# Kernel optimization log

Hardware: AMD Instinct MI355X
Metric: run time of the kernel (lower is better)

The kernel has to match this reference:

```python
import jax, jax.numpy as jnp
import numpy as np

DIM = 768
NUM_HEADS = 12
HEAD_DIM = DIM // NUM_HEADS
SCALE = HEAD_DIM ** -0.5  # qk_scale=None -> head_dim**-0.5


def setup_inputs() -> dict:
    key = jax.random.key(0)
    k1, k2, k3, k4 = jax.random.split(key, 4)
    B, N, C = 8, 1024, DIM
    x = jax.random.normal(k1, (B, N, C), dtype=jnp.float32)
    # qkv_bias=False -> no qkv bias; proj Linear has bias by default
    w_qkv = jax.random.normal(k2, (3 * C, C), dtype=jnp.float32) * (C ** -0.5)
    w_proj = jax.random.normal(k3, (C, C), dtype=jnp.float32) * (C ** -0.5)
    b_proj = jax.random.normal(k4, (C,), dtype=jnp.float32) * 0.02
    return {"x": x, "w_qkv": w_qkv, "w_proj": w_proj, "b_proj": b_proj}


def reference(x, w_qkv, w_proj, b_proj):
    B, N, C = x.shape
    H, D = NUM_HEADS, HEAD_DIM
    # qkv: [B,N,3C] -> [3,B,H,N,D]
    qkv = jnp.einsum('bnc,kc->bnk', x, w_qkv)
    qkv = qkv.reshape(B, N, 3, H, D).transpose(2, 0, 3, 1, 4)
    q, k, v = qkv[0], qkv[1], qkv[2]
    attn = jnp.einsum('bhnd,bhmd->bhnm', q, k) * SCALE
    attn = jax.nn.softmax(attn, axis=-1)  # attn_drop=0.0 -> identity
    out = jnp.einsum('bhnm,bhmd->bhnd', attn, v)
    out = out.transpose(0, 2, 1, 3).reshape(B, N, C)
    out = jnp.einsum('bnc,oc->bno', out, w_proj) + b_proj  # proj_drop=0.0
    return out
```

## Files before the change

### kernel.cpp

```cpp
#include <hip/hip_runtime.h>
#include <hip/hip_bf16.h>
#include <math.h>


typedef __bf16 bf16;
typedef __bf16 bf16x8 __attribute__((ext_vector_type(8)));
typedef __bf16 bf16x4 __attribute__((ext_vector_type(4)));
typedef float  f32x4  __attribute__((ext_vector_type(4)));
typedef short  s16x4  __attribute__((ext_vector_type(4)));

#define AS1 __attribute__((address_space(1)))
#define AS3 __attribute__((address_space(3)))

static __device__ __forceinline__ f32x4 mfma16x16x16bf16(s16x4 a, s16x4 b, f32x4 c) {
#if __has_builtin(__builtin_amdgcn_mfma_f32_16x16x16bf16_1k)
    return __builtin_amdgcn_mfma_f32_16x16x16bf16_1k(a, b, c, 0, 0, 0);
#else
    asm("v_mfma_f32_16x16x16_bf16 %0, %1, %2, %0" : "+v"(c) : "v"(a), "v"(b));
    return c;
#endif
}

__global__ void cvt3_f32_bf16(const float* __restrict__ s1, bf16* __restrict__ d1, int n1,
                              const float* __restrict__ s2, bf16* __restrict__ d2, int n2,
                              const float* __restrict__ s3, bf16* __restrict__ d3, int n3) {
    int i = blockIdx.x * blockDim.x + threadIdx.x;
    int stride = gridDim.x * blockDim.x;
    int total = n1 + n2 + n3;
    for (; i < total; i += stride) {
        const float* s; bf16* d; int k;
        if (i < n1)            { s = s1; d = d1; k = i; }
        else if (i < n1 + n2)  { s = s2; d = d2; k = i - n1; }
        else                   { s = s3; d = d3; k = i - n1 - n2; }
        f32x4 a = ((const f32x4*)s)[2 * (size_t)k];
        f32x4 bv = ((const f32x4*)s)[2 * (size_t)k + 1];
        bf16x8 o;
        o[0] = (bf16)a[0]; o[1] = (bf16)a[1]; o[2] = (bf16)a[2]; o[3] = (bf16)a[3];
        o[4] = (bf16)bv[0]; o[5] = (bf16)bv[1]; o[6] = (bf16)bv[2]; o[7] = (bf16)bv[3];
        ((bf16x8*)d)[k] = o;
    }
}

template <int EPI>
__launch_bounds__(256, 2)
__global__ void gemm_bt(const bf16* __restrict__ A, const bf16* __restrict__ Bw, int Kdim,
                        bf16* __restrict__ qo, bf16* __restrict__ ko, bf16* __restrict__ vto,
                        float* __restrict__ outf, const float* __restrict__ bias) {
    __shared__ alignas(16) bf16 As[2][128 * 64];
    __shared__ alignas(16) bf16 Bs[2][128 * 64];
    const int tid  = threadIdx.x;
    const int lane = tid & 63;
    const int wave = tid >> 6;
    const int lo = lane & 15, hi = lane >> 4;
    const int wr = wave >> 1, wc = wave & 1;
    const int m0 = blockIdx.x * 128;
    const int n0 = blockIdx.y * 128;

    const int s_phys = tid & 7;

    f32x4 acc[4][4] = {};

#define STAGE(buf, ks)                                                          \
    {                                                                           \
        _Pragma("unroll")                                                       \
        for (int i = 0; i < 4; ++i) {                                           \
            int row = ((i * 256 + tid) >> 3);                                   \
            int sl  = s_phys ^ (row & 7);                                       \
            __builtin_amdgcn_global_load_lds(                                   \
                (const AS1 void*)(A + (size_t)(m0 + row) * Kdim + (ks) * 64 + sl * 8), \
                (AS3 void*)(&As[buf][0] + (i * 256 + wave * 64) * 8), 16, 0, 0);\
            __builtin_amdgcn_global_load_lds(                                   \
                (const AS1 void*)(Bw + (size_t)(n0 + row) * Kdim + (ks) * 64 + sl * 8), \
                (AS3 void*)(&Bs[buf][0] + (i * 256 + wave * 64) * 8), 16, 0, 0);\
        }                                                                       \
    }

    const int KS = Kdim >> 6;
    STAGE(0, 0);
    __syncthreads();

    int cur = 0;
    for (int ks = 0; ks < KS; ++ks) {
        if (ks + 1 < KS) STAGE(cur ^ 1, ks + 1);

        bf16x8 af[4][2], bfr[4][2];
#pragma unroll
        for (int kk = 0; kk < 2; ++kk) {
            const int sl = ((kk << 2) | hi) ^ (lo & 7);
#pragma unroll
            for (int i = 0; i < 4; ++i)
                af[i][kk] = *(const bf16x8*)&As[cur][(wr * 64 + i * 16 + lo) * 64 + sl * 8];
#pragma unroll
            for (int j = 0; j < 4; ++j)
                bfr[j][kk] = *(const bf16x8*)&Bs[cur][(wc * 64 + j * 16 + lo) * 64 + sl * 8];
        }
#pragma unroll
        for (int i = 0; i < 4; ++i)
#pragma unroll
            for (int j = 0; j < 4; ++j) {
                acc[i][j] = __builtin_amdgcn_mfma_f32_16x16x32_bf16(af[i][0], bfr[j][0], acc[i][j], 0, 0, 0);
                acc[i][j] = __builtin_amdgcn_mfma_f32_16x16x32_bf16(af[i][1], bfr[j][1], acc[i][j], 0, 0, 0);
            }

        __syncthreads();
        cur ^= 1;
    }
#undef STAGE

    if (EPI == 0) {
        const int part = n0 / 768;
#pragma unroll
        for (int i = 0; i < 4; ++i) {
            int grow = m0 + wr * 64 + i * 16 + (hi << 2);
            int b = grow >> 10;
            int n = grow & 1023;
#pragma unroll
            for (int j = 0; j < 4; ++j) {
                int col = n0 + wc * 64 + j * 16 + lo;
                int rem = col - part * 768;
                int h = rem >> 6, d = rem & 63;
#pragma unroll
                for (int r = 0; r < 4; ++r) {
                    bf16 v = (bf16)acc[i][j][r];
                    int nn = n + r;
                    if (part == 0)
                        qo[((size_t)(b * 12 + h) * 1024 + nn) * 64 + d] = v;
                    else if (part == 1)
                        ko[((size_t)(b * 12 + h) * 1024 + nn) * 64 + d] = v;
                    else
                        vto[((size_t)(b * 12 + h) * 64 + d) * 1024 + nn] = v;
                }
            }
        }
    } else {
#pragma unroll
        for (int i = 0; i < 4; ++i) {
            int grow = m0 + wr * 64 + i * 16 + (hi << 2);
#pragma unroll
            for (int j = 0; j < 4; ++j) {
                int col = n0 + wc * 64 + j * 16 + lo;
                float bv = bias[col];
#pragma unroll
                for (int r = 0; r < 4; ++r)
                    outf[(size_t)(grow + r) * 768 + col] = acc[i][j][r] + bv;
            }
        }
    }
}

__launch_bounds__(256, 3)
__global__ void flash_attn(const bf16* __restrict__ qg, const bf16* __restrict__ kg,
                           const bf16* __restrict__ vtg, bf16* __restrict__ og) {
    __shared__ alignas(16) bf16 Ks[64 * 72];
    __shared__ alignas(16) bf16 Vts[64 * 72];

    const int tid = threadIdx.x, lane = tid & 63, wave = tid >> 6;
    const int lo = lane & 15, hi = lane >> 4;

    const int bid = blockIdx.x + (int)gridDim.x * blockIdx.y;
    const int xcd = bid & 7, idx = bid >> 3;
    const int head = xcd * 12 + (idx >> 3);
    const int q0 = (idx & 7) * 128;
    const int b = head / 12, h = head % 12;

    const size_t baseQK = (size_t)head * 1024 * 64;
    const size_t baseVt = (size_t)head * 64 * 1024;

    bf16x8 qf[2][2];
#pragma unroll
    for (int jq = 0; jq < 2; ++jq)
#pragma unroll
        for (int kk = 0; kk < 2; ++kk) {
            bf16x8 v = *(const bf16x8*)&qg[baseQK +
                (size_t)(q0 + wave * 32 + jq * 16 + lo) * 64 + kk * 32 + hi * 8];
#pragma unroll
            for (int e = 0; e < 8; ++e) v[e] = (bf16)((float)v[e] * 0.125f);
            qf[jq][kk] = v;
        }

    f32x4 of[4][2] = {};
    float lsum[2] = {0.f, 0.f};

    const int srow = tid >> 3;
    const int sc8  = (tid & 7) * 8;
    f32x4 kr[2], vr[2];

#pragma unroll
    for (int s = 0; s < 2; ++s) {
        kr[s] = *(const f32x4*)&kg[baseQK + (size_t)(srow + 32 * s) * 64 + sc8];
        vr[s] = *(const f32x4*)&vtg[baseVt + (size_t)(srow + 32 * s) * 1024 + sc8];
    }
#pragma unroll
    for (int s = 0; s < 2; ++s) {
        *(f32x4*)&Ks[(srow + 32 * s) * 72 + sc8]  = kr[s];
        *(f32x4*)&Vts[(srow + 32 * s) * 72 + sc8] = vr[s];
    }

    for (int t = 0; t < 16; ++t) {
        if (t + 1 < 16) {
#pragma unroll
            for (int s = 0; s < 2; ++s) {
                kr[s] = *(const f32x4*)&kg[baseQK +
                    (size_t)((t + 1) * 64 + srow + 32 * s) * 64 + sc8];
                vr[s] = *(const f32x4*)&vtg[baseVt +
                    (size_t)(srow + 32 * s) * 1024 + (t + 1) * 64 + sc8];
            }
        }
        __syncthreads();

        bf16x8 kf[4][2];
#pragma unroll
        for (int j = 0; j < 4; ++j)
#pragma unroll
            for (int kk = 0; kk < 2; ++kk)
                kf[j][kk] = *(const bf16x8*)&Ks[(j * 16 + lo) * 72 + kk * 32 + hi * 8];

        __builtin_amdgcn_s_setprio(1);
        f32x4 st[4][2];
#pragma unroll
        for (int j = 0; j < 4; ++j)
#pragma unroll
            for (int jq = 0; jq < 2; ++jq) {
                f32x4 z = {0.f, 0.f, 0.f, 0.f};
                z = __builtin_amdgcn_mfma_f32_16x16x32_bf16(kf[j][0], qf[jq][0], z, 0, 0, 0);
                st[j][jq] = __builtin_amdgcn_mfma_f32_16x16x32_bf16(kf[j][1], qf[jq][1], z, 0, 0, 0);
            }
        __builtin_amdgcn_s_setprio(0);

        s16x4 pb[4][2];
#pragma unroll
        for (int j = 0; j < 4; ++j)
#pragma unroll
            for (int jq = 0; jq < 2; ++jq) {
                f32x4 p;
#pragma unroll
                for (int r = 0; r < 4; ++r) p[r] = __expf(st[j][jq][r] - 10.0f);
                lsum[jq] += (p[0] + p[1]) + (p[2] + p[3]);
                bf16x4 pk;
#pragma unroll
                for (int r = 0; r < 4; ++r) pk[r] = (bf16)p[r];
                pb[j][jq] = __builtin_bit_cast(s16x4, pk);
            }

        __builtin_amdgcn_s_setprio(1);
#pragma unroll
        for (int jd = 0; jd < 4; ++jd) {
#pragma unroll
            for (int j = 0; j < 4; ++j) {
                s16x4 va = *(const s16x4*)&Vts[(jd * 16 + lo) * 72 + j * 16 + hi * 4];
#pragma unroll
                for (int jq = 0; jq < 2; ++jq)
                    of[jd][jq] = mfma16x16x16bf16(va, pb[j][jq], of[jd][jq]);
            }
        }
        __builtin_amdgcn_s_setprio(0);

        __syncthreads();
        if (t + 1 < 16) {
#pragma unroll
            for (int s = 0; s < 2; ++s) {
                *(f32x4*)&Ks[(srow + 32 * s) * 72 + sc8]  = kr[s];
                *(f32x4*)&Vts[(srow + 32 * s) * 72 + sc8] = vr[s];
            }
        }
    }

#pragma unroll
    for (int jq = 0; jq < 2; ++jq) {
        lsum[jq] += __shfl_xor(lsum[jq], 16);
        lsum[jq] += __shfl_xor(lsum[jq], 32);
    }

#pragma unroll
    for (int jq = 0; jq < 2; ++jq) {
        float rl = 1.0f / lsum[jq];
        int n = q0 + wave * 32 + jq * 16 + lo;
#pragma unroll
        for (int jd = 0; jd < 4; ++jd) {
            bf16x4 o;
#pragma unroll
            for (int r = 0; r < 4; ++r) o[r] = (bf16)(of[jd][jq][r] * rl);
            *(bf16x4*)&og[((size_t)b * 1024 + n) * 768 + h * 64 + jd * 16 + hi * 4] = o;
        }
    }
}

extern "C" void kernel_launch(void* const* d_in, const int* in_sizes, int n_in,
                              void* d_out, int out_size, void* d_ws, size_t ws_size,
                              hipStream_t stream) {
    const float* x      = (const float*)d_in[0];
    const float* w_qkv  = (const float*)d_in[1];
    const float* w_proj = (const float*)d_in[2];
    const float* b_proj = (const float*)d_in[3];
    float* out = (float*)d_out;

    bf16* xb     = (bf16*)d_ws;
    bf16* wqkvb  = xb + (size_t)8192 * 768;
    bf16* wprojb = wqkvb + (size_t)2304 * 768;
    bf16* qb     = wprojb + (size_t)768 * 768;
    bf16* kb     = qb + (size_t)96 * 1024 * 64;
    bf16* vtb    = kb + (size_t)96 * 1024 * 64;
    bf16* aob    = vtb + (size_t)96 * 1024 * 64;

    cvt3_f32_bf16<<<1024, 256, 0, stream>>>(x, xb, 8192 * 768 / 8,
                                            w_qkv, wqkvb, 2304 * 768 / 8,
                                            w_proj, wprojb, 768 * 768 / 8);

    gemm_bt<0><<<dim3(64, 18), 256, 0, stream>>>(xb, wqkvb, 768, qb, kb, vtb, nullptr, nullptr);
    flash_attn<<<dim3(8, 96), 256, 0, stream>>>(qb, kb, vtb, aob);
    gemm_bt<1><<<dim3(64, 6), 256, 0, stream>>>(aob, wprojb, 768, nullptr, nullptr, nullptr, out, b_proj);
}
```

Before: 200.4 us.

## Single-buffer GEMM LDS, raise occupancy, and remap blocks for XCD locality

The GEMM drops double-buffered shared memory in favour of a single buffer with a load-sync-compute-sync loop, halving LDS use so launch bounds can request four blocks per CU instead of two. The grid becomes 1D and block IDs are remapped so consecutive blocks on the same XCD share M-tiles, aiming for better L2 reuse. The cost is that global loads no longer overlap with MFMA work inside a block, so latency hiding now depends on having more resident blocks. The GY template parameter is unused.

```diff
diff --git a/kernel.cpp b/kernel.cpp
--- a/kernel.cpp
+++ b/kernel.cpp
@@ -41,26 +41,28 @@
     }
 }
 
-template <int EPI>
-__launch_bounds__(256, 2)
+template <int EPI, int GY>
+__launch_bounds__(256, 4)
 __global__ void gemm_bt(const bf16* __restrict__ A, const bf16* __restrict__ Bw, int Kdim,
                         bf16* __restrict__ qo, bf16* __restrict__ ko, bf16* __restrict__ vto,
                         float* __restrict__ outf, const float* __restrict__ bias) {
-    __shared__ alignas(16) bf16 As[2][128 * 64];
-    __shared__ alignas(16) bf16 Bs[2][128 * 64];
+    __shared__ alignas(16) bf16 As[128 * 64];
+    __shared__ alignas(16) bf16 Bs[128 * 64];
     const int tid  = threadIdx.x;
     const int lane = tid & 63;
     const int wave = tid >> 6;
     const int lo = lane & 15, hi = lane >> 4;
     const int wr = wave >> 1, wc = wave & 1;
-    const int m0 = blockIdx.x * 128;
-    const int n0 = blockIdx.y * 128;
+
+    const int bid = blockIdx.x;
+    const int xcd = bid & 7, idx = bid >> 3;
+    const int m0 = (xcd * 8 + (idx & 7)) * 128;
+    const int n0 = (idx >> 3) * 128;
 
     const int s_phys = tid & 7;
-
     f32x4 acc[4][4] = {};
 
-#define STAGE(buf, ks)                                                          \
+#define STAGE(ks)                                                               \
     {                                                                           \
         _Pragma("unroll")                                                       \
         for (int i = 0; i < 4; ++i) {                                           \
@@ -68,20 +70,17 @@
             int sl  = s_phys ^ (row & 7);                                       \
             __builtin_amdgcn_global_load_lds(                                   \
                 (const AS1 void*)(A + (size_t)(m0 + row) * Kdim + (ks) * 64 + sl * 8), \
-                (AS3 void*)(&As[buf][0] + (i * 256 + wave * 64) * 8), 16, 0, 0);\
+                (AS3 void*)(As + (i * 256 + wave * 64) * 8), 16, 0, 0);         \
             __builtin_amdgcn_global_load_lds(                                   \
                 (const AS1 void*)(Bw + (size_t)(n0 + row) * Kdim + (ks) * 64 + sl * 8), \
-                (AS3 void*)(&Bs[buf][0] + (i * 256 + wave * 64) * 8), 16, 0, 0);\
+                (AS3 void*)(Bs + (i * 256 + wave * 64) * 8), 16, 0, 0);         \
         }                                                                       \
     }
 
     const int KS = Kdim >> 6;
-    STAGE(0, 0);
-    __syncthreads();
-
-    int cur = 0;
     for (int ks = 0; ks < KS; ++ks) {
-        if (ks + 1 < KS) STAGE(cur ^ 1, ks + 1);
+        STAGE(ks);
+        __syncthreads();
 
         bf16x8 af[4][2], bfr[4][2];
 #pragma unroll
@@ -89,10 +88,10 @@
             const int sl = ((kk << 2) | hi) ^ (lo & 7);
 #pragma unroll
             for (int i = 0; i < 4; ++i)
-                af[i][kk] = *(const bf16x8*)&As[cur][(wr * 64 + i * 16 + lo) * 64 + sl * 8];
+                af[i][kk] = *(const bf16x8*)&As[(wr * 64 + i * 16 + lo) * 64 + sl * 8];
 #pragma unroll
             for (int j = 0; j < 4; ++j)
-                bfr[j][kk] = *(const bf16x8*)&Bs[cur][(wc * 64 + j * 16 + lo) * 64 + sl * 8];
+                bfr[j][kk] = *(const bf16x8*)&Bs[(wc * 64 + j * 16 + lo) * 64 + sl * 8];
         }
 #pragma unroll
         for (int i = 0; i < 4; ++i)
@@ -101,9 +100,7 @@
                 acc[i][j] = __builtin_amdgcn_mfma_f32_16x16x32_bf16(af[i][0], bfr[j][0], acc[i][j], 0, 0, 0);
                 acc[i][j] = __builtin_amdgcn_mfma_f32_16x16x32_bf16(af[i][1], bfr[j][1], acc[i][j], 0, 0, 0);
             }
-
         __syncthreads();
-        cur ^= 1;
     }
 #undef STAGE
 
@@ -306,7 +303,7 @@
                                             w_qkv, wqkvb, 2304 * 768 / 8,
                                             w_proj, wprojb, 768 * 768 / 8);
 
-    gemm_bt<0><<<dim3(64, 18), 256, 0, stream>>>(xb, wqkvb, 768, qb, kb, vtb, nullptr, nullptr);
+    gemm_bt<0, 18><<<64 * 18, 256, 0, stream>>>(xb, wqkvb, 768, qb, kb, vtb, nullptr, nullptr);
     flash_attn<<<dim3(8, 96), 256, 0, stream>>>(qb, kb, vtb, aob);
-    gemm_bt<1><<<dim3(64, 6), 256, 0, stream>>>(aob, wprojb, 768, nullptr, nullptr, nullptr, out, b_proj);
-}
+    gemm_bt<1, 6><<<64 * 6, 256, 0, stream>>>(aob, wprojb, 768, nullptr, nullptr, nullptr, out, b_proj);
+}
```

New measurement: 197.3 us. About the same (-1.6%).
